# Performance work log

Measured on AMD Instinct MI355X. Metric: run time of the kernel, lower is better.

## Reference

```python
import jax, jax.numpy as jnp
import numpy as np

N = 100000   # nodes
E = 1600000  # edges (avg degree 16)
D_IN = 128
HID = [128, 128]
D_OUT = 1


def _linear_params(key, in_c, out_c):
    k1, k2 = jax.random.split(key)
    s = 1.0 / np.sqrt(in_c)
    w = jax.random.uniform(k1, (out_c, in_c), jnp.float32, -s, s)
    b = jax.random.uniform(k2, (out_c,), jnp.float32, -s, s)
    return w, b


def setup_inputs() -> dict:
    key = jax.random.key(0)
    ks = jax.random.split(key, 16)
    inp = {}
    inp["x"] = jax.random.normal(ks[0], (N, D_IN), jnp.float32)
    inp["edge_index"] = jax.random.randint(ks[1], (2, E), 0, N, jnp.int32)
    # 3 GINConvs: dims (128->128), (128->128), (128->128); each MLP = Linear, ReLU, Linear
    dims = [(D_IN, HID[0]), (HID[0], HID[1]), (HID[1], HID[1])]
    for i, (ic, oc) in enumerate(dims):
        k1, k2 = jax.random.split(ks[2 + i])
        w1, b1 = _linear_params(k1, ic, oc)
        w2, b2 = _linear_params(k2, oc, oc)
        inp[f"c{i}_w1"], inp[f"c{i}_b1"] = w1, b1
        inp[f"c{i}_w2"], inp[f"c{i}_b2"] = w2, b2
        inp[f"c{i}_eps"] = jnp.zeros((), jnp.float32)  # train_eps=True, init 0
    last = HID[-1]
    inp["fc1_w"], inp["fc1_b"] = _linear_params(ks[8], last, last // 2)
    inp["fc2_w"], inp["fc2_b"] = _linear_params(ks[9], last // 2, D_OUT)
    return inp


def reference(x, edge_index,
              c0_w1, c0_b1, c0_w2, c0_b2, c0_eps,
              c1_w1, c1_b1, c1_w2, c1_b2, c1_eps,
              c2_w1, c2_b1, c2_w2, c2_b2, c2_eps,
              fc1_w, fc1_b, fc2_w, fc2_b):
    src, dst = edge_index[0], edge_index[1]  # messages flow src -> dst
    n = x.shape[0]

    def gin_conv(h, w1, b1, w2, b2, eps):
        # sum-aggregate neighbor features: scatter-add h[src] into dst
        agg = jax.ops.segment_sum(h[src], dst, num_segments=n)
        z = (1.0 + eps) * h + agg
        z = jax.nn.relu(z @ w1.T + b1) @ w2.T + b2  # GIN MLP
        return jax.nn.relu(z)  # outer ReLU in GINNet.forward

    h = gin_conv(x, c0_w1, c0_b1, c0_w2, c0_b2, c0_eps)
    h = gin_conv(h, c1_w1, c1_b1, c1_w2, c1_b2, c1_eps)
    h = gin_conv(h, c2_w1, c2_b1, c2_w2, c2_b2, c2_eps)
    h = jax.nn.relu(h @ fc1_w.T + fc1_b)
    return jax.nn.sigmoid(h @ fc2_w.T + fc2_b)
```

## Files before the change

kernel.cpp:

```cpp
#include <hip/hip_runtime.h>
#include <math.h>


using f16   = _Float16;
using f16x4 = __attribute__((ext_vector_type(4))) _Float16;
using f16x8 = __attribute__((ext_vector_type(8))) _Float16;
using f32x4 = __attribute__((ext_vector_type(4))) float;

constexpr int BINBLK = 256;

__device__ inline void glds16(const void* g, void* l) {
    __builtin_amdgcn_global_load_lds(
        (const __attribute__((address_space(1))) void*)g,
        (__attribute__((address_space(3))) void*)l, 16, 0, 0);
}


__global__ __launch_bounds__(512) void bucket_count_kernel(const int* __restrict__ dst,
                                                           int* __restrict__ cntM,
                                                           int E, int nbuck) {
    __shared__ int cnt[512];
    for (int i = threadIdx.x; i < nbuck; i += 512) cnt[i] = 0;
    __syncthreads();
    int chunk = (E + gridDim.x - 1) / gridDim.x;
    int lo = blockIdx.x * chunk, hi = min(lo + chunk, E);
    for (int e = lo + threadIdx.x; e < hi; e += 512)
        atomicAdd(&cnt[dst[e] >> 8], 1);
    __syncthreads();
    for (int i = threadIdx.x; i < nbuck; i += 512)
        cntM[(size_t)i * gridDim.x + blockIdx.x] = cnt[i];
}

__global__ __launch_bounds__(256) void scan_partial(const int* __restrict__ deg,
                                                    int* __restrict__ bsum, int n) {
    __shared__ int red[256];
    int b = blockIdx.x, t = threadIdx.x;
    int base = b * 1024;
    int s = 0;
#pragma unroll
    for (int j = 0; j < 4; ++j) {
        int idx = base + j * 256 + t;
        if (idx < n) s += deg[idx];
    }
    red[t] = s;
    __syncthreads();
    for (int d = 128; d > 0; d >>= 1) {
        if (t < d) red[t] += red[t + d];
        __syncthreads();
    }
    if (t == 0) bsum[b] = red[0];
}

__global__ __launch_bounds__(128) void scan_bsum(const int* __restrict__ bsum,
                                                 int* __restrict__ bbase, int nb,
                                                 int* __restrict__ total_out) {
    __shared__ int s[128];
    int t = threadIdx.x;
    s[t] = (t < nb) ? bsum[t] : 0;
    __syncthreads();
    for (int d = 1; d < 128; d <<= 1) {
        int v = (t >= d) ? s[t - d] : 0;
        __syncthreads();
        s[t] += v;
        __syncthreads();
    }
    bbase[t] = (t > 0) ? s[t - 1] : 0;
    if (t == 127) total_out[0] = s[127];
}

__global__ __launch_bounds__(256) void scan_final(const int* __restrict__ deg,
                                                  const int* __restrict__ bbase,
                                                  int* __restrict__ outA,
                                                  int* __restrict__ outB, int n) {
    __shared__ int red[256];
    int b = blockIdx.x, t = threadIdx.x;
    int base = b * 1024 + t * 4;
    int d0 = 0, d1 = 0, d2 = 0, d3 = 0;
    if (base + 3 < n) {
        int4 v = *(const int4*)&deg[base];
        d0 = v.x; d1 = v.y; d2 = v.z; d3 = v.w;
    } else {
        if (base < n) d0 = deg[base];
        if (base + 1 < n) d1 = deg[base + 1];
        if (base + 2 < n) d2 = deg[base + 2];
    }
    red[t] = d0 + d1 + d2 + d3;
    __syncthreads();
    for (int d = 1; d < 256; d <<= 1) {
        int v = (t >= d) ? red[t - d] : 0;
        __syncthreads();
        red[t] += v;
        __syncthreads();
    }
    int ex = bbase[b] + ((t > 0) ? red[t - 1] : 0);
    int o0 = ex, o1 = ex + d0, o2 = o1 + d1, o3 = o2 + d2;
    if (base + 3 < n) {
        *(int4*)&outA[base] = make_int4(o0, o1, o2, o3);
        *(int4*)&outB[base] = make_int4(o0, o1, o2, o3);
    } else {
        if (base < n) { outA[base] = o0; outB[base] = o0; }
        if (base + 1 < n) { outA[base + 1] = o1; outB[base + 1] = o1; }
        if (base + 2 < n) { outA[base + 2] = o2; outB[base + 2] = o2; }
    }
}

__global__ __launch_bounds__(512) void bin_kernel(const int* __restrict__ src,
                                                  const int* __restrict__ dst,
                                                  const int* __restrict__ baseM,
                                                  int2* __restrict__ stage, int E, int nbuck) {
    __shared__ int cur[512];
    for (int i = threadIdx.x; i < nbuck; i += 512)
        cur[i] = baseM[(size_t)i * gridDim.x + blockIdx.x];
    __syncthreads();
    int chunk = (E + gridDim.x - 1) / gridDim.x;
    int lo = blockIdx.x * chunk, hi = min(lo + chunk, E);
    for (int e = lo + threadIdx.x; e < hi; e += 512) {
        int d = dst[e];
        int p = atomicAdd(&cur[d >> 8], 1);
        stage[p] = make_int2(src[e], d);
    }
}

__global__ __launch_bounds__(256) void csr_kernel(const int2* __restrict__ stage,
                                                  const int* __restrict__ baseM,
                                                  int* __restrict__ offs,
                                                  int* __restrict__ col,
                                                  int E, int N, int nbuck, int binblk) {
    constexpr int CAP = 10240;
    __shared__ int cnt[256];
    __shared__ int sc[256];
    __shared__ int colbuf[CAP];
    int b = blockIdx.x, t = threadIdx.x;
    int base = baseM[(size_t)b * binblk];
    int end = (b + 1 < nbuck) ? baseM[(size_t)(b + 1) * binblk] : E;
    cnt[t] = 0;
    __syncthreads();
    for (int e = base + t; e < end; e += 256)
        atomicAdd(&cnt[stage[e].y & 255], 1);
    __syncthreads();
    int myCnt = cnt[t];
    sc[t] = myCnt;
    __syncthreads();
    for (int d = 1; d < 256; d <<= 1) {
        int u = (t >= d) ? sc[t - d] : 0;
        __syncthreads();
        sc[t] += u;
        __syncthreads();
    }
    int myExcl = sc[t] - myCnt;
    int node = b * 256 + t;
    if (node <= N) offs[node] = base + myExcl;
    cnt[t] = myExcl;
    __syncthreads();
    for (int e = base + t; e < end; e += 256) {
        int2 sd = stage[e];
        int p = atomicAdd(&cnt[sd.y & 255], 1);
        if (p < CAP) colbuf[p] = sd.x;
        else col[base + p] = sd.x;
    }
    __syncthreads();
    int lim = min(end - base, CAP);
    for (int i = t; i < lim; i += 256) col[base + i] = colbuf[i];
}

__global__ void cvt4_kernel(const float* __restrict__ in, f16* __restrict__ out, int nq) {
    int stride = gridDim.x * blockDim.x;
    for (int i = blockIdx.x * blockDim.x + threadIdx.x; i < nq; i += stride) {
        float4 v = *(const float4*)(in + (size_t)i * 4);
        f16x4 o = {(f16)v.x, (f16)v.y, (f16)v.z, (f16)v.w};
        *(f16x4*)(out + (size_t)i * 4) = o;
    }
}

struct CvtPack {
    const float* s[7];
    f16* d[7];
    int nq[7];
};
__global__ void cvt_pack_kernel(CvtPack p) {
    int seg = blockIdx.y;
    int nq = p.nq[seg];
    const float* in = p.s[seg];
    f16* out = p.d[seg];
    int stride = gridDim.x * blockDim.x;
    for (int i = blockIdx.x * blockDim.x + threadIdx.x; i < nq; i += stride) {
        float4 v = *(const float4*)(in + (size_t)i * 4);
        f16x4 o = {(f16)v.x, (f16)v.y, (f16)v.z, (f16)v.w};
        *(f16x4*)(out + (size_t)i * 4) = o;
    }
}

__global__ __launch_bounds__(256) void agg_kernel(const f16* __restrict__ h,
                                                  const int* __restrict__ offs,
                                                  const int* __restrict__ col,
                                                  const float* __restrict__ epsp,
                                                  f16* __restrict__ z, int n) {
    int node = blockIdx.x * 16 + (threadIdx.x >> 4);
    int li = threadIdx.x & 15;
    bool valid = node < n;
    int nd = valid ? node : (n - 1);
    const f16x8* hp = (const f16x8*)h;
    float e1 = 1.0f + epsp[0];
    f16x8 self = hp[(size_t)nd * 16 + li];
    float a[8];
#pragma unroll
    for (int c = 0; c < 8; ++c) a[c] = (float)self[c] * e1;
    int lo = offs[nd], hi = valid ? offs[nd + 1] : lo;

    int e = lo;
    for (; e + 8 <= hi; e += 8) {
        int idx[8];
#pragma unroll
        for (int j = 0; j < 8; ++j) idx[j] = col[e + j];
        f16x8 v[8];
#pragma unroll
        for (int j = 0; j < 8; ++j) v[j] = hp[(size_t)idx[j] * 16 + li];
#pragma unroll
        for (int j = 0; j < 8; ++j)
#pragma unroll
            for (int c = 0; c < 8; ++c) a[c] += (float)v[j][c];
    }
    if (e + 4 <= hi) {
        int idx[4];
#pragma unroll
        for (int j = 0; j < 4; ++j) idx[j] = col[e + j];
        f16x8 v[4];
#pragma unroll
        for (int j = 0; j < 4; ++j) v[j] = hp[(size_t)idx[j] * 16 + li];
#pragma unroll
        for (int j = 0; j < 4; ++j)
#pragma unroll
            for (int c = 0; c < 8; ++c) a[c] += (float)v[j][c];
        e += 4;
    }
    for (; e < hi; ++e) {
        f16x8 v = hp[(size_t)col[e] * 16 + li];
#pragma unroll
        for (int c = 0; c < 8; ++c) a[c] += (float)v[c];
    }
    if (valid) {
        f16x8 o;
#pragma unroll
        for (int c = 0; c < 8; ++c) o[c] = (f16)a[c];
        __builtin_nontemporal_store(o, (f16x8*)z + (size_t)nd * 16 + li);
    }
}

template <bool LAST>
__global__ __launch_bounds__(256) void conv_mlp_kernel(
    const f16* __restrict__ Z, const f16* __restrict__ W1f,
    const float* __restrict__ b1, const f16* __restrict__ W2f,
    const float* __restrict__ b2, f16* __restrict__ Hout, int M,
    const f16* __restrict__ fc1wf, const float* __restrict__ fc1b,
    const float* __restrict__ fc2w, const float* __restrict__ fc2b,
    float* __restrict__ out) {
    __shared__ __align__(16) f16 As[128 * 128];
    __shared__ __align__(16) f16 Ws[128 * 128];
    __shared__ float Red[LAST ? 128 * 17 : 1];

    const int tid = threadIdx.x;
    const int w = tid >> 6, lane = tid & 63;
    const int frow = lane & 15, kgrp = lane >> 4;
    const int m0 = blockIdx.x * 128;
    const int u = lane & 15, rsub = lane >> 4;

#pragma unroll
    for (int i = 0; i < 8; ++i) {
        int rowbase = (w * 8 + i) * 4;
        int r = rowbase + rsub;
        int gr = m0 + r;
        if (gr >= M) gr = M - 1;
        glds16(Z + (size_t)gr * 128 + ((u ^ (r & 7)) << 3), &As[rowbase * 128]);
    }
#pragma unroll
    for (int i = 0; i < 8; ++i) {
        int rowbase = (w * 8 + i) * 4;
        int r = rowbase + rsub;
        glds16(W1f + (size_t)r * 128 + ((u ^ (r & 7)) << 3), &Ws[rowbase * 128]);
    }
    __syncthreads();

    const int arow0 = w * 32 + frow;
    f32x4 acc[2][8];
#pragma unroll
    for (int mi = 0; mi < 2; ++mi)
#pragma unroll
        for (int nj = 0; nj < 8; ++nj) acc[mi][nj] = (f32x4){0.f, 0.f, 0.f, 0.f};

#pragma unroll
    for (int kk = 0; kk < 4; ++kk) {
        int kb = kk * 4 + kgrp;
        f16x8 a[2], b[8];
#pragma unroll
        for (int mi = 0; mi < 2; ++mi) {
            int r = arow0 + mi * 16;
            a[mi] = *(const f16x8*)&As[r * 128 + ((kb ^ (r & 7)) << 3)];
        }
#pragma unroll
        for (int nj = 0; nj < 8; ++nj) {
            int r = nj * 16 + frow;
            b[nj] = *(const f16x8*)&Ws[r * 128 + ((kb ^ (r & 7)) << 3)];
        }
#pragma unroll
        for (int mi = 0; mi < 2; ++mi)
#pragma unroll
            for (int nj = 0; nj < 8; ++nj)
                acc[mi][nj] = __builtin_amdgcn_mfma_f32_16x16x32_f16(a[mi], b[nj],
                                                                     acc[mi][nj], 0, 0, 0);
    }
    __syncthreads();

#pragma unroll
    for (int i = 0; i < 8; ++i) {
        int rowbase = (w * 8 + i) * 4;
        int r = rowbase + rsub;
        glds16(W2f + (size_t)r * 128 + ((u ^ (r & 7)) << 3), &Ws[rowbase * 128]);
    }
    {
        float bv[8];
#pragma unroll
        for (int nj = 0; nj < 8; ++nj) bv[nj] = b1[nj * 16 + frow];
#pragma unroll
        for (int mi = 0; mi < 2; ++mi)
#pragma unroll
            for (int nj = 0; nj < 8; ++nj) {
                int row0 = w * 32 + mi * 16 + kgrp * 4;
                int c = nj * 16 + frow;
                int cu = c >> 3, cl = c & 7;
#pragma unroll
                for (int r = 0; r < 4; ++r) {
                    int rr = row0 + r;
                    As[rr * 128 + ((cu ^ (rr & 7)) << 3) + cl] =
                        (f16)fmaxf(acc[mi][nj][r] + bv[nj], 0.f);
                }
            }
    }
    __syncthreads();

#pragma unroll
    for (int mi = 0; mi < 2; ++mi)
#pragma unroll
        for (int nj = 0; nj < 8; ++nj) acc[mi][nj] = (f32x4){0.f, 0.f, 0.f, 0.f};
#pragma unroll
    for (int kk = 0; kk < 4; ++kk) {
        int kb = kk * 4 + kgrp;
        f16x8 a[2], b[8];
#pragma unroll
        for (int mi = 0; mi < 2; ++mi) {
            int r = arow0 + mi * 16;
            a[mi] = *(const f16x8*)&As[r * 128 + ((kb ^ (r & 7)) << 3)];
        }
#pragma unroll
        for (int nj = 0; nj < 8; ++nj) {
            int r = nj * 16 + frow;
            b[nj] = *(const f16x8*)&Ws[r * 128 + ((kb ^ (r & 7)) << 3)];
        }
#pragma unroll
        for (int mi = 0; mi < 2; ++mi)
#pragma unroll
            for (int nj = 0; nj < 8; ++nj)
                acc[mi][nj] = __builtin_amdgcn_mfma_f32_16x16x32_f16(a[mi], b[nj],
                                                                     acc[mi][nj], 0, 0, 0);
    }

    float bv2[8];
#pragma unroll
    for (int nj = 0; nj < 8; ++nj) bv2[nj] = b2[nj * 16 + frow];

    if (!LAST) {
        __syncthreads();
#pragma unroll
        for (int mi = 0; mi < 2; ++mi)
#pragma unroll
            for (int nj = 0; nj < 8; ++nj) {
                int row0 = w * 32 + mi * 16 + kgrp * 4;
                int c = nj * 16 + frow;
#pragma unroll
                for (int r = 0; r < 4; ++r)
                    As[(row0 + r) * 128 + c] = (f16)fmaxf(acc[mi][nj][r] + bv2[nj], 0.f);
            }
        __syncthreads();
        for (int idx = tid; idx < 128 * 16; idx += 256) {
            int r = idx >> 4, q = idx & 15;
            int gm = m0 + r;
            if (gm < M)
                *(float4*)(Hout + (size_t)gm * 128 + q * 8) = *(const float4*)&As[r * 128 + q * 8];
        }
    } else {
        __syncthreads();
#pragma unroll
        for (int i = 0; i < 4; ++i) {
            int rowbase = (w * 4 + i) * 4;
            int r = rowbase + rsub;
            glds16(fc1wf + (size_t)r * 128 + ((u ^ (r & 7)) << 3), &Ws[rowbase * 128]);
        }
#pragma unroll
        for (int mi = 0; mi < 2; ++mi)
#pragma unroll
            for (int nj = 0; nj < 8; ++nj) {
                int row0 = w * 32 + mi * 16 + kgrp * 4;
                int c = nj * 16 + frow;
                int cu = c >> 3, cl = c & 7;
#pragma unroll
                for (int r = 0; r < 4; ++r) {
                    int rr = row0 + r;
                    As[rr * 128 + ((cu ^ (rr & 7)) << 3) + cl] =
                        (f16)fmaxf(acc[mi][nj][r] + bv2[nj], 0.f);
                }
            }
        __syncthreads();

        f32x4 acc3[2][4];
#pragma unroll
        for (int mi = 0; mi < 2; ++mi)
#pragma unroll
            for (int nj = 0; nj < 4; ++nj) acc3[mi][nj] = (f32x4){0.f, 0.f, 0.f, 0.f};
#pragma unroll
        for (int kk = 0; kk < 4; ++kk) {
            int kb = kk * 4 + kgrp;
            f16x8 a[2], b[4];
#pragma unroll
            for (int mi = 0; mi < 2; ++mi) {
                int r = arow0 + mi * 16;
                a[mi] = *(const f16x8*)&As[r * 128 + ((kb ^ (r & 7)) << 3)];
            }
#pragma unroll
            for (int nj = 0; nj < 4; ++nj) {
                int r = nj * 16 + frow;
                b[nj] = *(const f16x8*)&Ws[r * 128 + ((kb ^ (r & 7)) << 3)];
            }
#pragma unroll
            for (int mi = 0; mi < 2; ++mi)
#pragma unroll
                for (int nj = 0; nj < 4; ++nj)
                    acc3[mi][nj] = __builtin_amdgcn_mfma_f32_16x16x32_f16(a[mi], b[nj],
                                                                          acc3[mi][nj], 0, 0, 0);
        }
        float bvf[4], f2[4];
#pragma unroll
        for (int nj = 0; nj < 4; ++nj) {
            bvf[nj] = fc1b[nj * 16 + frow];
            f2[nj] = fc2w[nj * 16 + frow];
        }
        float part[2][4];
#pragma unroll
        for (int mi = 0; mi < 2; ++mi)
#pragma unroll
            for (int r = 0; r < 4; ++r) part[mi][r] = 0.f;
#pragma unroll
        for (int mi = 0; mi < 2; ++mi)
#pragma unroll
            for (int nj = 0; nj < 4; ++nj)
#pragma unroll
                for (int r = 0; r < 4; ++r)
                    part[mi][r] += fmaxf(acc3[mi][nj][r] + bvf[nj], 0.f) * f2[nj];
#pragma unroll
        for (int mi = 0; mi < 2; ++mi)
#pragma unroll
            for (int r = 0; r < 4; ++r)
                Red[(w * 32 + mi * 16 + kgrp * 4 + r) * 17 + frow] = part[mi][r];
        __syncthreads();
        if (tid < 128) {
            float s = fc2b[0];
#pragma unroll
            for (int q = 0; q < 16; ++q) s += Red[tid * 17 + q];
            int m = m0 + tid;
            if (m < M) out[m] = 1.f / (1.f + expf(-s));
        }
    }
}

extern "C" void kernel_launch(void* const* d_in, const int* in_sizes, int n_in,
                              void* d_out, int out_size, void* d_ws, size_t ws_size,
                              hipStream_t stream) {
    const float* x = (const float*)d_in[0];
    const int* ei = (const int*)d_in[1];
    const int N = in_sizes[0] / 128;
    const int E = in_sizes[1] / 2;
    const int* srcIdx = ei;
    const int* dstIdx = ei + E;

    const float* w1[3] = {(const float*)d_in[2], (const float*)d_in[7], (const float*)d_in[12]};
    const float* b1[3] = {(const float*)d_in[3], (const float*)d_in[8], (const float*)d_in[13]};
    const float* w2[3] = {(const float*)d_in[4], (const float*)d_in[9], (const float*)d_in[14]};
    const float* b2[3] = {(const float*)d_in[5], (const float*)d_in[10], (const float*)d_in[15]};
    const float* eps[3] = {(const float*)d_in[6], (const float*)d_in[11], (const float*)d_in[16]};
    const float* fc1w = (const float*)d_in[17];
    const float* fc1b = (const float*)d_in[18];
    const float* fc2w = (const float*)d_in[19];
    const float* fc2b = (const float*)d_in[20];

    char* ws = (char*)d_ws;
    size_t p = 0;
    auto carve = [&](size_t bytes) -> char* {
        char* r = ws + p;
        p = (p + bytes + 255) & ~(size_t)255;
        return r;
    };
    const int nbuck = (N + 255) >> 8;
    const int nm = nbuck * BINBLK;
    int* offs = (int*)carve((size_t)(N + 1) * 4);
    int* col = (int*)carve((size_t)E * 4);
    int* cntM = (int*)carve((size_t)nm * 4);
    int* baseM = (int*)carve((size_t)nm * 4);
    int* baseM2 = (int*)carve((size_t)nm * 4);
    int* bsum = (int*)carve(128 * 4);
    int* bbase = (int*)carve(128 * 4);
    int* tot = (int*)carve(4);
    int2* stage = (int2*)carve((size_t)E * 8);
    f16* H0 = (f16*)carve((size_t)N * 128 * 2);
    f16* H1 = (f16*)carve((size_t)N * 128 * 2);
    f16* Z = (f16*)carve((size_t)N * 128 * 2);
    f16* w1f[3], *w2f[3];
    for (int i = 0; i < 3; ++i) {
        w1f[i] = (f16*)carve(128 * 128 * 2);
        w2f[i] = (f16*)carve(128 * 128 * 2);
    }
    f16* fc1wf = (f16*)carve(64 * 128 * 2);
    (void)ws_size;

    const int SB2 = (nm + 1023) / 1024;
    bucket_count_kernel<<<BINBLK, 512, 0, stream>>>(dstIdx, cntM, E, nbuck);
    scan_partial<<<SB2, 256, 0, stream>>>(cntM, bsum, nm);
    scan_bsum<<<1, 128, 0, stream>>>(bsum, bbase, SB2, tot);
    scan_final<<<SB2, 256, 0, stream>>>(cntM, bbase, baseM, baseM2, nm);
    bin_kernel<<<BINBLK, 512, 0, stream>>>(srcIdx, dstIdx, baseM, stage, E, nbuck);
    csr_kernel<<<nbuck, 256, 0, stream>>>(stage, baseM, offs, col, E, N, nbuck, BINBLK);

    cvt4_kernel<<<2048, 256, 0, stream>>>(x, H0, N * 128 / 4);
    CvtPack cp;
    for (int i = 0; i < 3; ++i) {
        cp.s[i] = w1[i];     cp.d[i] = w1f[i];     cp.nq[i] = 128 * 128 / 4;
        cp.s[3 + i] = w2[i]; cp.d[3 + i] = w2f[i]; cp.nq[3 + i] = 128 * 128 / 4;
    }
    cp.s[6] = fc1w; cp.d[6] = fc1wf; cp.nq[6] = 64 * 128 / 4;
    cvt_pack_kernel<<<dim3(16, 7), 256, 0, stream>>>(cp);

    const int aggGrid = (N + 15) / 16;
    const int gemmGrid = (N + 127) / 128;

    agg_kernel<<<aggGrid, 256, 0, stream>>>(H0, offs, col, eps[0], Z, N);
    conv_mlp_kernel<false><<<gemmGrid, 256, 0, stream>>>(
        Z, w1f[0], b1[0], w2f[0], b2[0], H1, N, nullptr, nullptr, nullptr, nullptr, nullptr);
    agg_kernel<<<aggGrid, 256, 0, stream>>>(H1, offs, col, eps[1], Z, N);
    conv_mlp_kernel<false><<<gemmGrid, 256, 0, stream>>>(
        Z, w1f[1], b1[1], w2f[1], b2[1], H0, N, nullptr, nullptr, nullptr, nullptr, nullptr);
    agg_kernel<<<aggGrid, 256, 0, stream>>>(H0, offs, col, eps[2], Z, N);
    conv_mlp_kernel<true><<<gemmGrid, 256, 0, stream>>>(
        Z, w1f[2], b1[2], w2f[2], b2[2], nullptr, N, fc1wf, fc1b, fc2w, fc2b, (float*)d_out);
}
```

Before: 296.5 us.

## Stage CSR column indices in LDS and process 32 nodes per aggregation block

The aggregation kernel now loads each block's contiguous range of CSR column indices into shared memory once, with a global fallback when the range is too large. Each node is handled by 8 lanes making two passes over the 16 feature chunks, so one block covers 32 nodes. This is meant to cut the repeated global index loads that each lane previously issued. In exchange it adds two barriers, extra LDS use, and halves the lanes per node, which serialises the feature chunks and lowers memory-level parallelism on the neighbour gathers.

```diff
diff --git a/kernel.cpp b/kernel.cpp
--- a/kernel.cpp
+++ b/kernel.cpp
@@ -195,54 +195,78 @@
                                                   const int* __restrict__ col,
                                                   const float* __restrict__ epsp,
                                                   f16* __restrict__ z, int n) {
-    int node = blockIdx.x * 16 + (threadIdx.x >> 4);
-    int li = threadIdx.x & 15;
-    bool valid = node < n;
-    int nd = valid ? node : (n - 1);
+    __shared__ int colLDS[2048];
+    __shared__ int sOffs[33];
+    const int tid = threadIdx.x;
+    const int nb = blockIdx.x * 32;
+    if (tid < 33) sOffs[tid] = offs[min(nb + tid, n)];
+    __syncthreads();
+    const int base = sOffs[0];
+    const int len = sOffs[32] - base;
+    const bool useLds = len <= 2048;
+    if (useLds) {
+        for (int i = tid; i < len; i += 256)
+            colLDS[i] = __builtin_nontemporal_load(&col[base + i]);
+    }
+    __syncthreads();
+
+    const int grp = tid >> 3;
+    const int li = tid & 7;
+    const int node = nb + grp;
+    const bool valid = node < n;
+    const int nd = valid ? node : (n - 1);
+    const int lo = sOffs[grp] - base;
+    const int hi = valid ? (sOffs[grp + 1] - base) : lo;
     const f16x8* hp = (const f16x8*)h;
-    float e1 = 1.0f + epsp[0];
-    f16x8 self = hp[(size_t)nd * 16 + li];
-    float a[8];
-#pragma unroll
-    for (int c = 0; c < 8; ++c) a[c] = (float)self[c] * e1;
-    int lo = offs[nd], hi = valid ? offs[nd + 1] : lo;
-
-    int e = lo;
-    for (; e + 8 <= hi; e += 8) {
-        int idx[8];
-#pragma unroll
-        for (int j = 0; j < 8; ++j) idx[j] = col[e + j];
-        f16x8 v[8];
-#pragma unroll
-        for (int j = 0; j < 8; ++j) v[j] = hp[(size_t)idx[j] * 16 + li];
-#pragma unroll
-        for (int j = 0; j < 8; ++j)
-#pragma unroll
-            for (int c = 0; c < 8; ++c) a[c] += (float)v[j][c];
-    }
-    if (e + 4 <= hi) {
-        int idx[4];
-#pragma unroll
-        for (int j = 0; j < 4; ++j) idx[j] = col[e + j];
-        f16x8 v[4];
-#pragma unroll
-        for (int j = 0; j < 4; ++j) v[j] = hp[(size_t)idx[j] * 16 + li];
-#pragma unroll
-        for (int j = 0; j < 4; ++j)
-#pragma unroll
-            for (int c = 0; c < 8; ++c) a[c] += (float)v[j][c];
-        e += 4;
-    }
-    for (; e < hi; ++e) {
-        f16x8 v = hp[(size_t)col[e] * 16 + li];
-#pragma unroll
-        for (int c = 0; c < 8; ++c) a[c] += (float)v[c];
-    }
-    if (valid) {
-        f16x8 o;
-#pragma unroll
-        for (int c = 0; c < 8; ++c) o[c] = (f16)a[c];
-        __builtin_nontemporal_store(o, (f16x8*)z + (size_t)nd * 16 + li);
+    const float e1 = 1.0f + epsp[0];
+
+#pragma unroll
+    for (int ph = 0; ph < 2; ++ph) {
+        const int co = ph * 8 + li;
+        f16x8 self = hp[(size_t)nd * 16 + co];
+        float a[8];
+#pragma unroll
+        for (int c = 0; c < 8; ++c) a[c] = (float)self[c] * e1;
+        int e = lo;
+        for (; e + 8 <= hi; e += 8) {
+            int idx[8];
+#pragma unroll
+            for (int j = 0; j < 8; ++j)
+                idx[j] = useLds ? colLDS[e + j] : col[base + e + j];
+            f16x8 v[8];
+#pragma unroll
+            for (int j = 0; j < 8; ++j) v[j] = hp[(size_t)idx[j] * 16 + co];
+#pragma unroll
+            for (int j = 0; j < 8; ++j)
+#pragma unroll
+                for (int c = 0; c < 8; ++c) a[c] += (float)v[j][c];
+        }
+        if (e + 4 <= hi) {
+            int idx[4];
+#pragma unroll
+            for (int j = 0; j < 4; ++j)
+                idx[j] = useLds ? colLDS[e + j] : col[base + e + j];
+            f16x8 v[4];
+#pragma unroll
+            for (int j = 0; j < 4; ++j) v[j] = hp[(size_t)idx[j] * 16 + co];
+#pragma unroll
+            for (int j = 0; j < 4; ++j)
+#pragma unroll
+                for (int c = 0; c < 8; ++c) a[c] += (float)v[j][c];
+            e += 4;
+        }
+        for (; e < hi; ++e) {
+            int idx = useLds ? colLDS[e] : col[base + e];
+            f16x8 v = hp[(size_t)idx * 16 + co];
+#pragma unroll
+            for (int c = 0; c < 8; ++c) a[c] += (float)v[c];
+        }
+        if (valid) {
+            f16x8 o;
+#pragma unroll
+            for (int c = 0; c < 8; ++c) o[c] = (f16)a[c];
+            __builtin_nontemporal_store(o, (f16x8*)z + (size_t)nd * 16 + co);
+        }
     }
 }
 
@@ -536,7 +560,7 @@
     cp.s[6] = fc1w; cp.d[6] = fc1wf; cp.nq[6] = 64 * 128 / 4;
     cvt_pack_kernel<<<dim3(16, 7), 256, 0, stream>>>(cp);
 
-    const int aggGrid = (N + 15) / 16;
+    const int aggGrid = (N + 31) / 32;
     const int gemmGrid = (N + 127) / 128;
 
     agg_kernel<<<aggGrid, 256, 0, stream>>>(H0, offs, col, eps[0], Z, N);
```

After: 289.3 us. 1.03x faster.
